# Kernel optimization log

Measured on AMD Instinct MI355X. Metric: run time of the kernel, lower is better.

Reference implementation:

```python
import jax, jax.numpy as jnp
import numpy as np

B, N, D, H, O = 4096, 128, 64, 256, 128  # batch, memory_size, memory_dim, controller_dim, output_size


def setup_inputs() -> dict:
    key = jax.random.key(0)
    ks = jax.random.split(key, 20)
    s = 0.05
    inp = {
        "x": jax.random.normal(ks[0], (B, O), jnp.float32),
        "memory": jax.random.normal(ks[1], (B, N, D), jnp.float32),
        "h": jax.random.normal(ks[2], (B, H), jnp.float32),
        "c": jax.random.normal(ks[3], (B, H), jnp.float32),
        # LSTMCell params (torch layout: gates ordered i, f, g, o; input = x||read_vec of width O+D)
        "W_ih": jax.random.normal(ks[4], (4 * H, O + D), jnp.float32) * s,
        "W_hh": jax.random.normal(ks[5], (4 * H, H), jnp.float32) * s,
        "b_ih": jax.random.normal(ks[6], (4 * H,), jnp.float32) * s,
        "b_hh": jax.random.normal(ks[7], (4 * H,), jnp.float32) * s,
        "W_read": jax.random.normal(ks[8], (N, H), jnp.float32) * s,
        "b_read": jax.random.normal(ks[9], (N,), jnp.float32) * s,
        "W_write": jax.random.normal(ks[10], (N, H), jnp.float32) * s,
        "b_write": jax.random.normal(ks[11], (N,), jnp.float32) * s,
        "W_erase": jax.random.normal(ks[12], (D, H), jnp.float32) * s,
        "b_erase": jax.random.normal(ks[13], (D,), jnp.float32) * s,
        "W_add": jax.random.normal(ks[14], (D, H), jnp.float32) * s,
        "b_add": jax.random.normal(ks[15], (D,), jnp.float32) * s,
        "W_out": jax.random.normal(ks[16], (O, H + D), jnp.float32) * s,
        "b_out": jax.random.normal(ks[17], (O,), jnp.float32) * s,
    }
    return inp


def reference(x, memory, h, c, W_ih, W_hh, b_ih, b_hh, W_read, b_read,
              W_write, b_write, W_erase, b_erase, W_add, b_add, W_out, b_out):
    # read: softmax attention over memory rows, addressed by previous hidden state
    read_w = jax.nn.softmax(h @ W_read.T + b_read, axis=-1)          # [B, N]
    read_vec = jnp.einsum("bn,bnd->bd", read_w, memory)               # [B, D]

    # LSTMCell step (torch gate order: i, f, g, o)
    ctrl_in = jnp.concatenate([x, read_vec], axis=-1)                 # [B, O+D]
    gates = ctrl_in @ W_ih.T + b_ih + h @ W_hh.T + b_hh               # [B, 4H]
    i, f, g, o = jnp.split(gates, 4, axis=-1)
    i, f, o = jax.nn.sigmoid(i), jax.nn.sigmoid(f), jax.nn.sigmoid(o)
    g = jnp.tanh(g)
    c_new = f * c + i * g
    h_new = o * jnp.tanh(c_new)

    # write: outer-product erase/add update
    write_w = jax.nn.softmax(h_new @ W_write.T + b_write, axis=-1)    # [B, N]
    erase = jax.nn.sigmoid(h_new @ W_erase.T + b_erase)               # [B, D]
    add = jnp.tanh(h_new @ W_add.T + b_add)                           # [B, D]
    ww = write_w[:, :, None]                                          # [B, N, 1]
    mem_new = memory * (1.0 - ww * erase[:, None, :]) + ww * add[:, None, :]

    out = jnp.concatenate([h_new, read_vec], axis=-1) @ W_out.T + b_out  # [B, O]
    return (out, mem_new, h_new, c_new)
```

## Files before the change

kernel.cpp:

```cpp
#include <hip/hip_runtime.h>
#include <math.h>


typedef __attribute__((ext_vector_type(8))) short bf16x8;
typedef __attribute__((ext_vector_type(4))) float f32x4;
typedef __attribute__((ext_vector_type(4))) unsigned short us4;

#define MFMA16(a, b, c) __builtin_amdgcn_mfma_f32_16x16x32_bf16(a, b, c, 0, 0, 0)
#define GLL16(gp, lp) __builtin_amdgcn_global_load_lds( \
    (const __attribute__((address_space(1))) void*)(gp), \
    (__attribute__((address_space(3))) void*)(lp), 16, 0, 0)
#define SW(row, s) ((s) ^ ((row) & 3))

__device__ __forceinline__ float sigf(float v) { return 1.f / (1.f + __expf(-v)); }

__device__ __forceinline__ unsigned short f2bf(float f) {
    unsigned u = __builtin_bit_cast(unsigned, f);
    u = (u + 0x7FFFu + ((u >> 16) & 1u)) >> 16;
    return (unsigned short)u;
}

__global__ __launch_bounds__(256) void p_pack(
    const float* __restrict__ Wih, const float* __restrict__ Whh,
    const float* __restrict__ bih, const float* __restrict__ bhh,
    const float* __restrict__ Wr, const float* __restrict__ Ww,
    const float* __restrict__ We, const float* __restrict__ Wa,
    const float* __restrict__ bw, const float* __restrict__ be,
    const float* __restrict__ ba, const float* __restrict__ Wo,
    const float* __restrict__ x, const float* __restrict__ h,
    unsigned short* __restrict__ Wg, float* __restrict__ bsum,
    unsigned short* __restrict__ Wr_b, unsigned short* __restrict__ Wh_b,
    float* __restrict__ bh_b, unsigned short* __restrict__ Wo_b,
    unsigned short* __restrict__ Ag)
{
    int idx = blockIdx.x * 256 + threadIdx.x;
    int stride = gridDim.x * 256;
    for (int i = idx; i < 1024 * 448; i += stride) {
        int r = i / 448, cc = i - r * 448;
        float v = (cc < 192) ? Wih[(size_t)r * 192 + cc] : Whh[(size_t)r * 256 + (cc - 192)];
        Wg[i] = f2bf(v);
    }
    for (int i = idx; i < 1024; i += stride) bsum[i] = bih[i] + bhh[i];
    for (int i = idx; i < 128 * 256; i += stride) Wr_b[i] = f2bf(Wr[i]);
    for (int i = idx; i < 256 * 256; i += stride) {
        int r = i >> 8, cc = i & 255;
        float v = (r < 128) ? Ww[(size_t)r * 256 + cc]
                : (r < 192) ? We[(size_t)(r - 128) * 256 + cc]
                            : Wa[(size_t)(r - 192) * 256 + cc];
        Wh_b[i] = f2bf(v);
    }
    for (int i = idx; i < 256; i += stride)
        bh_b[i] = (i < 128) ? bw[i] : (i < 192 ? be[i - 128] : ba[i - 192]);
    for (int i = idx; i < 128 * 320; i += stride) Wo_b[i] = f2bf(Wo[i]);
    for (int i = idx; i < 4096 * 96; i += stride) {
        int row = i / 96, j = i - row * 96;
        float4 v = (j < 32) ? ((const float4*)(x + (size_t)row * 128))[j]
                            : ((const float4*)(h + (size_t)row * 256))[j - 32];
        us4 o = { f2bf(v.x), f2bf(v.y), f2bf(v.z), f2bf(v.w) };
        int col = (j < 32) ? j * 4 : 192 + (j - 32) * 4;
        *(us4*)(Ag + (size_t)row * 448 + col) = o;
    }
}

__global__ __launch_bounds__(128) void k1_read_attn(
    const unsigned short* __restrict__ Ag, const unsigned short* __restrict__ Wr_b,
    const float* __restrict__ br, float* __restrict__ read_w)
{
    __shared__ unsigned short As[32 * 32];
    __shared__ unsigned short Bs[128 * 32];
    int t = threadIdx.x;
    int wid = t >> 6, lane = t & 63;
    int cl = lane & 15, ks = lane >> 4;
    int b0 = blockIdx.x * 32;

    int arow = t >> 2;
    const unsigned short* aSrc = Ag + (size_t)(b0 + arow) * 448 + 192 + SW(arow, t & 3) * 8;
    unsigned short* aDst = As + wid * 512;
    const unsigned short* bSrc[4];
    unsigned short* bDst[4];
#pragma unroll
    for (int J = 0; J < 4; ++J) {
        int rJ = J * 32 + (t >> 2);
        bSrc[J] = Wr_b + (size_t)rJ * 256 + SW(rJ, t & 3) * 8;
        bDst[J] = Bs + J * 1024 + wid * 512;
    }

    int mr = wid * 16 + cl;
    int aOff = mr * 32 + SW(mr, ks) * 8;
    int bOff[8];
#pragma unroll
    for (int f = 0; f < 8; ++f) { int br_ = f * 16 + cl; bOff[f] = br_ * 32 + SW(br_, ks) * 8; }

    f32x4 acc[8] = {};
    for (int kc = 0; kc < 8; ++kc) {
        __syncthreads();
        GLL16(aSrc, aDst);
#pragma unroll
        for (int J = 0; J < 4; ++J) GLL16(bSrc[J], bDst[J]);
        aSrc += 32;
#pragma unroll
        for (int J = 0; J < 4; ++J) bSrc[J] += 32;
        __syncthreads();
        bf16x8 a = *(const bf16x8*)(As + aOff);
#pragma unroll
        for (int f = 0; f < 8; ++f)
            acc[f] = MFMA16(a, *(const bf16x8*)(Bs + bOff[f]), acc[f]);
    }

    float bb[8];
#pragma unroll
    for (int f = 0; f < 8; ++f) bb[f] = br[f * 16 + cl];
#pragma unroll
    for (int r = 0; r < 4; ++r) {
        int row = b0 + wid * 16 + ks * 4 + r;
        float v[8];
#pragma unroll
        for (int f = 0; f < 8; ++f) v[f] = acc[f][r] + bb[f];
        float m = v[0];
#pragma unroll
        for (int f = 1; f < 8; ++f) m = fmaxf(m, v[f]);
#pragma unroll
        for (int mk = 8; mk >= 1; mk >>= 1) m = fmaxf(m, __shfl_xor(m, mk));
        float s = 0.f;
#pragma unroll
        for (int f = 0; f < 8; ++f) { v[f] = __expf(v[f] - m); s += v[f]; }
#pragma unroll
        for (int mk = 8; mk >= 1; mk >>= 1) s += __shfl_xor(s, mk);
        float inv = 1.f / s;
#pragma unroll
        for (int f = 0; f < 8; ++f)
            read_w[(size_t)row * 128 + f * 16 + cl] = v[f] * inv;
    }
}

__global__ __launch_bounds__(256) void k2_read_vec(
    const float* __restrict__ mem, const float* __restrict__ read_w,
    unsigned short* __restrict__ Ag, unsigned short* __restrict__ Aout)
{
    __shared__ float part[16][68];
    int t = threadIdx.x;
    int b = blockIdx.x;
    int np = t >> 4, d4 = t & 15;
    const float4* m4 = (const float4*)(mem + (size_t)b * 8192);
    float4 acc = make_float4(0.f, 0.f, 0.f, 0.f);
#pragma unroll
    for (int j = 0; j < 8; ++j) {
        int n = np + 16 * j;
        float w = read_w[(size_t)b * 128 + n];
        float4 mv = m4[t + 256 * j];
        acc.x += w * mv.x; acc.y += w * mv.y; acc.z += w * mv.z; acc.w += w * mv.w;
    }
    part[np][d4 * 4 + 0] = acc.x; part[np][d4 * 4 + 1] = acc.y;
    part[np][d4 * 4 + 2] = acc.z; part[np][d4 * 4 + 3] = acc.w;
    __syncthreads();
    if (t < 64) {
        float s = 0.f;
#pragma unroll
        for (int q = 0; q < 16; ++q) s += part[q][t];
        unsigned short bv = f2bf(s);
        Ag[(size_t)b * 448 + 128 + t] = bv;
        Aout[(size_t)b * 320 + 256 + t] = bv;
    }
}

__global__ __launch_bounds__(256) void k3_gates_mfma(
    const unsigned short* __restrict__ Ag, const unsigned short* __restrict__ Wg,
    const float* __restrict__ bsum, const float* __restrict__ c,
    float* __restrict__ h_new, float* __restrict__ c_new,
    unsigned short* __restrict__ Aout)
{
    __shared__ unsigned short As[64 * 32];
    __shared__ unsigned short Bs[256 * 32];
    int t = threadIdx.x;
    int wid = t >> 6, lane = t & 63;
    int cl = lane & 15, ks = lane >> 4;
    int b0 = blockIdx.x * 64;
    int u0 = blockIdx.y * 64;

    int arow = t >> 2;
    const unsigned short* aSrc = Ag + (size_t)(b0 + arow) * 448 + SW(arow, t & 3) * 8;
    unsigned short* aDst = As + wid * 512;
    const unsigned short* bSrc[4];
    unsigned short* bDst[4];
#pragma unroll
    for (int j = 0; j < 4; ++j) {
        int i = j * 256 + t;
        int rl = i >> 2;
        int g = rl >> 6, u = rl & 63;
        bSrc[j] = Wg + (size_t)(g * 256 + u0 + u) * 448 + SW(rl, t & 3) * 8;
        bDst[j] = Bs + (j * 256 + wid * 64) * 8;
    }

    int aOff[4];
#pragma unroll
    for (int rf = 0; rf < 4; ++rf) {
        int mr = rf * 16 + cl;
        aOff[rf] = mr * 32 + SW(mr, ks) * 8;
    }
    int bOff[4];
#pragma unroll
    for (int g = 0; g < 4; ++g) {
        int br_ = g * 64 + wid * 16 + cl;
        bOff[g] = br_ * 32 + SW(br_, ks) * 8;
    }

    f32x4 acc[4][4] = {};
    for (int kc = 0; kc < 14; ++kc) {
        __syncthreads();
        GLL16(aSrc, aDst);
        GLL16(bSrc[0], bDst[0]); GLL16(bSrc[1], bDst[1]);
        GLL16(bSrc[2], bDst[2]); GLL16(bSrc[3], bDst[3]);
        aSrc += 32;
#pragma unroll
        for (int j = 0; j < 4; ++j) bSrc[j] += 32;
        __syncthreads();
        bf16x8 a[4], b[4];
#pragma unroll
        for (int rf = 0; rf < 4; ++rf) a[rf] = *(const bf16x8*)(As + aOff[rf]);
#pragma unroll
        for (int g = 0; g < 4; ++g) b[g] = *(const bf16x8*)(Bs + bOff[g]);
#pragma unroll
        for (int rf = 0; rf < 4; ++rf)
#pragma unroll
            for (int g = 0; g < 4; ++g)
                acc[rf][g] = MFMA16(a[rf], b[g], acc[rf][g]);
    }

    int unit = u0 + wid * 16 + cl;
    float bi = bsum[unit], bf_ = bsum[256 + unit];
    float bg = bsum[512 + unit], bo_ = bsum[768 + unit];
#pragma unroll
    for (int rf = 0; rf < 4; ++rf) {
#pragma unroll
        for (int r = 0; r < 4; ++r) {
            int row = b0 + rf * 16 + ks * 4 + r;
            float iv = sigf(acc[rf][0][r] + bi);
            float fv = sigf(acc[rf][1][r] + bf_);
            float gv = tanhf(acc[rf][2][r] + bg);
            float ov = sigf(acc[rf][3][r] + bo_);
            float cv = fv * c[(size_t)row * 256 + unit] + iv * gv;
            float hv = ov * tanhf(cv);
            c_new[(size_t)row * 256 + unit] = cv;
            h_new[(size_t)row * 256 + unit] = hv;
            Aout[(size_t)row * 320 + unit] = f2bf(hv);
        }
    }
}

__global__ __launch_bounds__(256) void k46_heads_out(
    const unsigned short* __restrict__ Aout, const unsigned short* __restrict__ Wh_b,
    const unsigned short* __restrict__ Wo_b, const float* __restrict__ bh_b,
    const float* __restrict__ bo, float* __restrict__ write_w,
    float* __restrict__ erase, float* __restrict__ addv, float* __restrict__ outp)
{
    __shared__ unsigned short As[32 * 32];
    __shared__ unsigned short Bh[256 * 32];
    __shared__ unsigned short Bo[128 * 32];
    int t = threadIdx.x;
    int wid = t >> 6, lane = t & 63;
    int cl = lane & 15, ks = lane >> 4;
    int rf = wid >> 1, ch = wid & 1;
    int b0 = blockIdx.x * 32;

    int arow = t >> 2;
    const unsigned short* aSrc = Aout + (size_t)(b0 + (arow & 31)) * 320 + SW(arow & 31, t & 3) * 8;
    unsigned short* aDst = As + (wid & 1) * 512;
    const unsigned short* bhSrc[4];
    unsigned short* bhDst[4];
#pragma unroll
    for (int j = 0; j < 4; ++j) {
        int rl = (j * 256 + t) >> 2;
        bhSrc[j] = Wh_b + (size_t)rl * 256 + SW(rl, t & 3) * 8;
        bhDst[j] = Bh + (j * 256 + wid * 64) * 8;
    }
    const unsigned short* boSrc[2];
    unsigned short* boDst[2];
#pragma unroll
    for (int j = 0; j < 2; ++j) {
        int rj = j * 64 + (t >> 2);
        boSrc[j] = Wo_b + (size_t)rj * 320 + SW(rj, t & 3) * 8;
        boDst[j] = Bo + j * 2048 + wid * 512;
    }

    int mr = rf * 16 + cl;
    int aOff = mr * 32 + SW(mr, ks) * 8;
    int bOffH[8], bOffO[4];
#pragma unroll
    for (int f = 0; f < 8; ++f) { int br_ = (ch * 8 + f) * 16 + cl; bOffH[f] = br_ * 32 + SW(br_, ks) * 8; }
#pragma unroll
    for (int f = 0; f < 4; ++f) { int br_ = (ch * 4 + f) * 16 + cl; bOffO[f] = br_ * 32 + SW(br_, ks) * 8; }

    f32x4 accH[8] = {};
    f32x4 accO[4] = {};
    for (int kc = 0; kc < 10; ++kc) {
        __syncthreads();
        if (t < 128) GLL16(aSrc, aDst);
        if (kc < 8) {
            GLL16(bhSrc[0], bhDst[0]); GLL16(bhSrc[1], bhDst[1]);
            GLL16(bhSrc[2], bhDst[2]); GLL16(bhSrc[3], bhDst[3]);
        }
        GLL16(boSrc[0], boDst[0]); GLL16(boSrc[1], boDst[1]);
        aSrc += 32;
#pragma unroll
        for (int j = 0; j < 4; ++j) bhSrc[j] += 32;
#pragma unroll
        for (int j = 0; j < 2; ++j) boSrc[j] += 32;
        __syncthreads();
        bf16x8 a = *(const bf16x8*)(As + aOff);
        if (kc < 8) {
#pragma unroll
            for (int f = 0; f < 8; ++f)
                accH[f] = MFMA16(a, *(const bf16x8*)(Bh + bOffH[f]), accH[f]);
        }
#pragma unroll
        for (int f = 0; f < 4; ++f)
            accO[f] = MFMA16(a, *(const bf16x8*)(Bo + bOffO[f]), accO[f]);
    }

    float bbh[8], bbo[4];
#pragma unroll
    for (int f = 0; f < 8; ++f) bbh[f] = bh_b[(ch * 8 + f) * 16 + cl];
#pragma unroll
    for (int f = 0; f < 4; ++f) bbo[f] = bo[ch * 64 + f * 16 + cl];

#pragma unroll
    for (int r = 0; r < 4; ++r) {
        int row = b0 + rf * 16 + ks * 4 + r;
        if (ch == 0) {
            float v[8];
#pragma unroll
            for (int f = 0; f < 8; ++f) v[f] = accH[f][r] + bbh[f];
            float m = v[0];
#pragma unroll
            for (int f = 1; f < 8; ++f) m = fmaxf(m, v[f]);
#pragma unroll
            for (int mk = 8; mk >= 1; mk >>= 1) m = fmaxf(m, __shfl_xor(m, mk));
            float s = 0.f;
#pragma unroll
            for (int f = 0; f < 8; ++f) { v[f] = __expf(v[f] - m); s += v[f]; }
#pragma unroll
            for (int mk = 8; mk >= 1; mk >>= 1) s += __shfl_xor(s, mk);
            float inv = 1.f / s;
#pragma unroll
            for (int f = 0; f < 8; ++f)
                write_w[(size_t)row * 128 + f * 16 + cl] = v[f] * inv;
        } else {
#pragma unroll
            for (int f = 0; f < 4; ++f)
                erase[(size_t)row * 64 + f * 16 + cl] = sigf(accH[f][r] + bbh[f]);
#pragma unroll
            for (int f = 4; f < 8; ++f)
                addv[(size_t)row * 64 + (f - 4) * 16 + cl] = tanhf(accH[f][r] + bbh[f]);
        }
#pragma unroll
        for (int f = 0; f < 4; ++f)
            outp[(size_t)row * 128 + ch * 64 + f * 16 + cl] = accO[f][r] + bbo[f];
    }
}

__global__ __launch_bounds__(256) void k5_mem_update(
    const float* __restrict__ mem, const float* __restrict__ write_w,
    const float* __restrict__ erase, const float* __restrict__ addv,
    float* __restrict__ mem_new)
{
    int t = threadIdx.x; int b = blockIdx.x;
    int np = t >> 4, d0 = (t & 15) * 4;
    const f32x4* m4 = (const f32x4*)(mem + (size_t)b * 8192);
    f32x4* o4 = (f32x4*)(mem_new + (size_t)b * 8192);
    f32x4 e4 = *(const f32x4*)(erase + (size_t)b * 64 + d0);
    f32x4 a4 = *(const f32x4*)(addv + (size_t)b * 64 + d0);
#pragma unroll
    for (int j = 0; j < 8; ++j) {
        int n = np + 16 * j;
        float w = write_w[(size_t)b * 128 + n];
        f32x4 m = m4[t + 256 * j];
        f32x4 r;
        r[0] = m[0] * (1.f - w * e4[0]) + w * a4[0];
        r[1] = m[1] * (1.f - w * e4[1]) + w * a4[1];
        r[2] = m[2] * (1.f - w * e4[2]) + w * a4[2];
        r[3] = m[3] * (1.f - w * e4[3]) + w * a4[3];
        __builtin_nontemporal_store(r, &o4[t + 256 * j]);
    }
}

extern "C" void kernel_launch(void* const* d_in, const int* in_sizes, int n_in,
                              void* d_out, int out_size, void* d_ws, size_t ws_size,
                              hipStream_t stream)
{
    const float* x    = (const float*)d_in[0];
    const float* mem  = (const float*)d_in[1];
    const float* h    = (const float*)d_in[2];
    const float* c    = (const float*)d_in[3];
    const float* Wih  = (const float*)d_in[4];
    const float* Whh  = (const float*)d_in[5];
    const float* bih  = (const float*)d_in[6];
    const float* bhh  = (const float*)d_in[7];
    const float* Wr   = (const float*)d_in[8];
    const float* br   = (const float*)d_in[9];
    const float* Ww   = (const float*)d_in[10];
    const float* bw   = (const float*)d_in[11];
    const float* We   = (const float*)d_in[12];
    const float* be   = (const float*)d_in[13];
    const float* Wa   = (const float*)d_in[14];
    const float* ba   = (const float*)d_in[15];
    const float* Wo   = (const float*)d_in[16];
    const float* bo   = (const float*)d_in[17];

    float* out     = (float*)d_out;
    float* mem_new = out + 524288;
    float* h_new   = out + 34078720;
    float* c_new   = out + 35127296;

    float* ws      = (float*)d_ws;
    float* read_w  = ws;
    float* write_w = ws + 524288;
    float* erase   = ws + 1048576;
    float* addv    = ws + 1310720;
    float* bsum    = ws + 1572864;
    float* bh_b    = ws + 1573888;
    unsigned short* ub   = (unsigned short*)(ws + 1574144);
    unsigned short* Ag   = ub;
    unsigned short* Aout = ub + 1835008;
    unsigned short* Wg   = ub + 3145728;
    unsigned short* Wr_b = ub + 3604480;
    unsigned short* Wh_b = ub + 3637248;
    unsigned short* Wo_b = ub + 3702784;

    p_pack<<<512, 256, 0, stream>>>(Wih, Whh, bih, bhh, Wr, Ww, We, Wa, bw, be, ba, Wo,
                                    x, h, Wg, bsum, Wr_b, Wh_b, bh_b, Wo_b, Ag);
    k1_read_attn<<<128, 128, 0, stream>>>(Ag, Wr_b, br, read_w);
    k2_read_vec<<<4096, 256, 0, stream>>>(mem, read_w, Ag, Aout);
    k3_gates_mfma<<<dim3(64, 4), 256, 0, stream>>>(Ag, Wg, bsum, c, h_new, c_new, Aout);
    k46_heads_out<<<128, 256, 0, stream>>>(Aout, Wh_b, Wo_b, bh_b, bo,
                                           write_w, erase, addv, out);
    k5_mem_update<<<4096, 256, 0, stream>>>(mem, write_w, erase, addv, mem_new);
}
```

Baseline: 110.6 us.

## Fuse six kernels into three: prep+read attention, gates, heads+memory update

```diff
diff --git a/kernel.cpp b/kernel.cpp
--- a/kernel.cpp
+++ b/kernel.cpp
@@ -20,20 +20,32 @@
     return (unsigned short)u;
 }
 
-__global__ __launch_bounds__(256) void p_pack(
+__global__ __launch_bounds__(256) void kA_prep(
     const float* __restrict__ Wih, const float* __restrict__ Whh,
     const float* __restrict__ bih, const float* __restrict__ bhh,
-    const float* __restrict__ Wr, const float* __restrict__ Ww,
-    const float* __restrict__ We, const float* __restrict__ Wa,
-    const float* __restrict__ bw, const float* __restrict__ be,
-    const float* __restrict__ ba, const float* __restrict__ Wo,
-    const float* __restrict__ x, const float* __restrict__ h,
+    const float* __restrict__ Wr, const float* __restrict__ br,
+    const float* __restrict__ Ww, const float* __restrict__ We,
+    const float* __restrict__ Wa, const float* __restrict__ bw,
+    const float* __restrict__ be, const float* __restrict__ ba,
+    const float* __restrict__ Wo, const float* __restrict__ x,
+    const float* __restrict__ h, const float* __restrict__ mem,
     unsigned short* __restrict__ Wg, float* __restrict__ bsum,
-    unsigned short* __restrict__ Wr_b, unsigned short* __restrict__ Wh_b,
-    float* __restrict__ bh_b, unsigned short* __restrict__ Wo_b,
-    unsigned short* __restrict__ Ag)
+    unsigned short* __restrict__ Wh_b, float* __restrict__ bh_b,
+    unsigned short* __restrict__ Wo_b, unsigned short* __restrict__ Ag,
+    unsigned short* __restrict__ Aout)
 {
-    int idx = blockIdx.x * 256 + threadIdx.x;
+    __shared__ unsigned short As[16 * 32];
+    __shared__ unsigned short Bs[128 * 32];
+    __shared__ float sc[16][128];
+    __shared__ float wL[16][128];
+    __shared__ float part[16][68];
+
+    int t = threadIdx.x;
+    int wid = t >> 6, lane = t & 63;
+    int cl = lane & 15, ks = lane >> 4;
+    int b0 = blockIdx.x * 16;
+
+    int idx = blockIdx.x * 256 + t;
     int stride = gridDim.x * 256;
     for (int i = idx; i < 1024 * 448; i += stride) {
         int r = i / 448, cc = i - r * 448;
@@ -41,7 +53,6 @@
         Wg[i] = f2bf(v);
     }
     for (int i = idx; i < 1024; i += stride) bsum[i] = bih[i] + bhh[i];
-    for (int i = idx; i < 128 * 256; i += stride) Wr_b[i] = f2bf(Wr[i]);
     for (int i = idx; i < 256 * 256; i += stride) {
         int r = i >> 8, cc = i & 255;
         float v = (r < 128) ? Ww[(size_t)r * 256 + cc]
@@ -60,110 +71,102 @@
         int col = (j < 32) ? j * 4 : 192 + (j - 32) * 4;
         *(us4*)(Ag + (size_t)row * 448 + col) = o;
     }
-}
-
-__global__ __launch_bounds__(128) void k1_read_attn(
-    const unsigned short* __restrict__ Ag, const unsigned short* __restrict__ Wr_b,
-    const float* __restrict__ br, float* __restrict__ read_w)
-{
-    __shared__ unsigned short As[32 * 32];
-    __shared__ unsigned short Bs[128 * 32];
-    int t = threadIdx.x;
-    int wid = t >> 6, lane = t & 63;
-    int cl = lane & 15, ks = lane >> 4;
-    int b0 = blockIdx.x * 32;
-
-    int arow = t >> 2;
-    const unsigned short* aSrc = Ag + (size_t)(b0 + arow) * 448 + 192 + SW(arow, t & 3) * 8;
-    unsigned short* aDst = As + wid * 512;
-    const unsigned short* bSrc[4];
-    unsigned short* bDst[4];
-#pragma unroll
-    for (int J = 0; J < 4; ++J) {
-        int rJ = J * 32 + (t >> 2);
-        bSrc[J] = Wr_b + (size_t)rJ * 256 + SW(rJ, t & 3) * 8;
-        bDst[J] = Bs + J * 1024 + wid * 512;
-    }
-
-    int mr = wid * 16 + cl;
-    int aOff = mr * 32 + SW(mr, ks) * 8;
-    int bOff[8];
-#pragma unroll
-    for (int f = 0; f < 8; ++f) { int br_ = f * 16 + cl; bOff[f] = br_ * 32 + SW(br_, ks) * 8; }
-
-    f32x4 acc[8] = {};
+
+    int aOff = cl * 32 + SW(cl, ks) * 8;
+    int bOff[4];
+#pragma unroll
+    for (int f = 0; f < 4; ++f) {
+        int br_ = (wid * 4 + f) * 16 + cl;
+        bOff[f] = br_ * 32 + SW(br_, ks) * 8;
+    }
+    f32x4 acc[4] = {};
     for (int kc = 0; kc < 8; ++kc) {
         __syncthreads();
-        GLL16(aSrc, aDst);
-#pragma unroll
-        for (int J = 0; J < 4; ++J) GLL16(bSrc[J], bDst[J]);
-        aSrc += 32;
-#pragma unroll
-        for (int J = 0; J < 4; ++J) bSrc[J] += 32;
-        __syncthreads();
-        bf16x8 a = *(const bf16x8*)(As + aOff);
-#pragma unroll
-        for (int f = 0; f < 8; ++f)
-            acc[f] = MFMA16(a, *(const bf16x8*)(Bs + bOff[f]), acc[f]);
-    }
-
-    float bb[8];
-#pragma unroll
-    for (int f = 0; f < 8; ++f) bb[f] = br[f * 16 + cl];
-#pragma unroll
-    for (int r = 0; r < 4; ++r) {
-        int row = b0 + wid * 16 + ks * 4 + r;
+        {
+            int row = t >> 4, k0 = (t & 15) * 2;
+            float2 hv = *(const float2*)(h + (size_t)(b0 + row) * 256 + kc * 32 + k0);
+            unsigned pk = (unsigned)f2bf(hv.x) | ((unsigned)f2bf(hv.y) << 16);
+            *(unsigned*)(As + row * 32 + SW(row, k0 >> 3) * 8 + (k0 & 7)) = pk;
+        }
+        {
+            int row = t >> 1, k0 = (t & 1) * 16;
+            const float4* wp = (const float4*)(Wr + (size_t)row * 256 + kc * 32 + k0);
+            float4 w0 = wp[0], w1 = wp[1], w2 = wp[2], w3 = wp[3];
+            us4 p0 = { f2bf(w0.x), f2bf(w0.y), f2bf(w0.z), f2bf(w0.w) };
+            us4 p1 = { f2bf(w1.x), f2bf(w1.y), f2bf(w1.z), f2bf(w1.w) };
+            us4 p2 = { f2bf(w2.x), f2bf(w2.y), f2bf(w2.z), f2bf(w2.w) };
+            us4 p3 = { f2bf(w3.x), f2bf(w3.y), f2bf(w3.z), f2bf(w3.w) };
+            int g0 = k0 >> 3;
+            unsigned short* basep = Bs + row * 32;
+            *(us4*)(basep + SW(row, g0) * 8)     = p0;
+            *(us4*)(basep + SW(row, g0) * 8 + 4) = p1;
+            *(us4*)(basep + SW(row, g0 + 1) * 8)     = p2;
+            *(us4*)(basep + SW(row, g0 + 1) * 8 + 4) = p3;
+        }
+        __syncthreads();
+        if (wid < 2) {
+            bf16x8 a = *(const bf16x8*)(As + aOff);
+#pragma unroll
+            for (int f = 0; f < 4; ++f)
+                acc[f] = MFMA16(a, *(const bf16x8*)(Bs + bOff[f]), acc[f]);
+        }
+    }
+    if (wid < 2) {
+#pragma unroll
+        for (int f = 0; f < 4; ++f)
+#pragma unroll
+            for (int r = 0; r < 4; ++r)
+                sc[ks * 4 + r][(wid * 4 + f) * 16 + cl] = acc[f][r];
+    }
+    __syncthreads();
+    {
+        int row = t >> 4, l = t & 15;
         float v[8];
 #pragma unroll
-        for (int f = 0; f < 8; ++f) v[f] = acc[f][r] + bb[f];
+        for (int j = 0; j < 8; ++j) v[j] = sc[row][l + 16 * j] + br[l + 16 * j];
         float m = v[0];
 #pragma unroll
-        for (int f = 1; f < 8; ++f) m = fmaxf(m, v[f]);
+        for (int j = 1; j < 8; ++j) m = fmaxf(m, v[j]);
 #pragma unroll
         for (int mk = 8; mk >= 1; mk >>= 1) m = fmaxf(m, __shfl_xor(m, mk));
         float s = 0.f;
 #pragma unroll
-        for (int f = 0; f < 8; ++f) { v[f] = __expf(v[f] - m); s += v[f]; }
+        for (int j = 0; j < 8; ++j) { v[j] = __expf(v[j] - m); s += v[j]; }
 #pragma unroll
         for (int mk = 8; mk >= 1; mk >>= 1) s += __shfl_xor(s, mk);
         float inv = 1.f / s;
 #pragma unroll
-        for (int f = 0; f < 8; ++f)
-            read_w[(size_t)row * 128 + f * 16 + cl] = v[f] * inv;
+        for (int j = 0; j < 8; ++j) wL[row][l + 16 * j] = v[j] * inv;
+    }
+    __syncthreads();
+
+    int np = t >> 4, d4 = t & 15;
+    for (int r = 0; r < 16; ++r) {
+        int row = b0 + r;
+        const f32x4* m4 = (const f32x4*)(mem + (size_t)row * 8192);
+        f32x4 a4 = { 0.f, 0.f, 0.f, 0.f };
+#pragma unroll
+        for (int j = 0; j < 8; ++j) {
+            float w = wL[r][np + 16 * j];
+            f32x4 mv = m4[t + 256 * j];
+            a4 += w * mv;
+        }
+        part[np][d4 * 4 + 0] = a4[0]; part[np][d4 * 4 + 1] = a4[1];
+        part[np][d4 * 4 + 2] = a4[2]; part[np][d4 * 4 + 3] = a4[3];
+        __syncthreads();
+        if (t < 64) {
+            float s = 0.f;
+#pragma unroll
+            for (int q = 0; q < 16; ++q) s += part[q][t];
+            unsigned short bv = f2bf(s);
+            Ag[(size_t)row * 448 + 128 + t] = bv;
+            Aout[(size_t)row * 320 + 256 + t] = bv;
+        }
+        __syncthreads();
     }
 }
 
-__global__ __launch_bounds__(256) void k2_read_vec(
-    const float* __restrict__ mem, const float* __restrict__ read_w,
-    unsigned short* __restrict__ Ag, unsigned short* __restrict__ Aout)
-{
-    __shared__ float part[16][68];
-    int t = threadIdx.x;
-    int b = blockIdx.x;
-    int np = t >> 4, d4 = t & 15;
-    const float4* m4 = (const float4*)(mem + (size_t)b * 8192);
-    float4 acc = make_float4(0.f, 0.f, 0.f, 0.f);
-#pragma unroll
-    for (int j = 0; j < 8; ++j) {
-        int n = np + 16 * j;
-        float w = read_w[(size_t)b * 128 + n];
-        float4 mv = m4[t + 256 * j];
-        acc.x += w * mv.x; acc.y += w * mv.y; acc.z += w * mv.z; acc.w += w * mv.w;
-    }
-    part[np][d4 * 4 + 0] = acc.x; part[np][d4 * 4 + 1] = acc.y;
-    part[np][d4 * 4 + 2] = acc.z; part[np][d4 * 4 + 3] = acc.w;
-    __syncthreads();
-    if (t < 64) {
-        float s = 0.f;
-#pragma unroll
-        for (int q = 0; q < 16; ++q) s += part[q][t];
-        unsigned short bv = f2bf(s);
-        Ag[(size_t)b * 448 + 128 + t] = bv;
-        Aout[(size_t)b * 320 + 256 + t] = bv;
-    }
-}
-
-__global__ __launch_bounds__(256) void k3_gates_mfma(
+__global__ __launch_bounds__(256) void kB_gates(
     const unsigned short* __restrict__ Ag, const unsigned short* __restrict__ Wg,
     const float* __restrict__ bsum, const float* __restrict__ c,
     float* __restrict__ h_new, float* __restrict__ c_new,
@@ -184,8 +187,7 @@
     unsigned short* bDst[4];
 #pragma unroll
     for (int j = 0; j < 4; ++j) {
-        int i = j * 256 + t;
-        int rl = i >> 2;
+        int rl = (j * 256 + t) >> 2;
         int g = rl >> 6, u = rl & 63;
         bSrc[j] = Wg + (size_t)(g * 256 + u0 + u) * 448 + SW(rl, t & 3) * 8;
         bDst[j] = Bs + (j * 256 + wid * 64) * 8;
@@ -247,24 +249,26 @@
     }
 }
 
-__global__ __launch_bounds__(256) void k46_heads_out(
+__global__ __launch_bounds__(256) void kC_heads_out_mem(
     const unsigned short* __restrict__ Aout, const unsigned short* __restrict__ Wh_b,
     const unsigned short* __restrict__ Wo_b, const float* __restrict__ bh_b,
-    const float* __restrict__ bo, float* __restrict__ write_w,
-    float* __restrict__ erase, float* __restrict__ addv, float* __restrict__ outp)
+    const float* __restrict__ bo, const float* __restrict__ mem,
+    float* __restrict__ outp, float* __restrict__ mem_new)
 {
-    __shared__ unsigned short As[32 * 32];
+    __shared__ unsigned short As[16 * 32];
     __shared__ unsigned short Bh[256 * 32];
     __shared__ unsigned short Bo[128 * 32];
+    __shared__ float sc[16][256];
+    __shared__ __align__(16) float wL[16][128];
+    __shared__ __align__(16) float eL[16][64];
+    __shared__ __align__(16) float aL[16][64];
+
     int t = threadIdx.x;
     int wid = t >> 6, lane = t & 63;
     int cl = lane & 15, ks = lane >> 4;
-    int rf = wid >> 1, ch = wid & 1;
-    int b0 = blockIdx.x * 32;
-
-    int arow = t >> 2;
-    const unsigned short* aSrc = Aout + (size_t)(b0 + (arow & 31)) * 320 + SW(arow & 31, t & 3) * 8;
-    unsigned short* aDst = As + (wid & 1) * 512;
+    int b0 = blockIdx.x * 16;
+
+    const unsigned short* aSrc = Aout + (size_t)(b0 + (lane >> 2)) * 320 + SW(lane >> 2, lane & 3) * 8;
     const unsigned short* bhSrc[4];
     unsigned short* bhDst[4];
 #pragma unroll
@@ -282,19 +286,18 @@
         boDst[j] = Bo + j * 2048 + wid * 512;
     }
 
-    int mr = rf * 16 + cl;
-    int aOff = mr * 32 + SW(mr, ks) * 8;
-    int bOffH[8], bOffO[4];
-#pragma unroll
-    for (int f = 0; f < 8; ++f) { int br_ = (ch * 8 + f) * 16 + cl; bOffH[f] = br_ * 32 + SW(br_, ks) * 8; }
-#pragma unroll
-    for (int f = 0; f < 4; ++f) { int br_ = (ch * 4 + f) * 16 + cl; bOffO[f] = br_ * 32 + SW(br_, ks) * 8; }
-
-    f32x4 accH[8] = {};
-    f32x4 accO[4] = {};
+    int aOff = cl * 32 + SW(cl, ks) * 8;
+    int bOffH[4], bOffO[2];
+#pragma unroll
+    for (int f = 0; f < 4; ++f) { int br_ = (wid * 4 + f) * 16 + cl; bOffH[f] = br_ * 32 + SW(br_, ks) * 8; }
+#pragma unroll
+    for (int f = 0; f < 2; ++f) { int br_ = (wid * 2 + f) * 16 + cl; bOffO[f] = br_ * 32 + SW(br_, ks) * 8; }
+
+    f32x4 accH[4] = {};
+    f32x4 accO[2] = {};
     for (int kc = 0; kc < 10; ++kc) {
         __syncthreads();
-        if (t < 128) GLL16(aSrc, aDst);
+        if (t < 64) GLL16(aSrc, As);
         if (kc < 8) {
             GLL16(bhSrc[0], bhDst[0]); GLL16(bhSrc[1], bhDst[1]);
             GLL16(bhSrc[2], bhDst[2]); GLL16(bhSrc[3], bhDst[3]);
@@ -309,77 +312,74 @@
         bf16x8 a = *(const bf16x8*)(As + aOff);
         if (kc < 8) {
 #pragma unroll
-            for (int f = 0; f < 8; ++f)
+            for (int f = 0; f < 4; ++f)
                 accH[f] = MFMA16(a, *(const bf16x8*)(Bh + bOffH[f]), accH[f]);
         }
 #pragma unroll
-        for (int f = 0; f < 4; ++f)
+        for (int f = 0; f < 2; ++f)
             accO[f] = MFMA16(a, *(const bf16x8*)(Bo + bOffO[f]), accO[f]);
     }
 
-    float bbh[8], bbo[4];
-#pragma unroll
-    for (int f = 0; f < 8; ++f) bbh[f] = bh_b[(ch * 8 + f) * 16 + cl];
-#pragma unroll
-    for (int f = 0; f < 4; ++f) bbo[f] = bo[ch * 64 + f * 16 + cl];
-
-#pragma unroll
-    for (int r = 0; r < 4; ++r) {
-        int row = b0 + rf * 16 + ks * 4 + r;
-        if (ch == 0) {
-            float v[8];
-#pragma unroll
-            for (int f = 0; f < 8; ++f) v[f] = accH[f][r] + bbh[f];
-            float m = v[0];
-#pragma unroll
-            for (int f = 1; f < 8; ++f) m = fmaxf(m, v[f]);
-#pragma unroll
-            for (int mk = 8; mk >= 1; mk >>= 1) m = fmaxf(m, __shfl_xor(m, mk));
-            float s = 0.f;
-#pragma unroll
-            for (int f = 0; f < 8; ++f) { v[f] = __expf(v[f] - m); s += v[f]; }
-#pragma unroll
-            for (int mk = 8; mk >= 1; mk >>= 1) s += __shfl_xor(s, mk);
-            float inv = 1.f / s;
-#pragma unroll
-            for (int f = 0; f < 8; ++f)
-                write_w[(size_t)row * 128 + f * 16 + cl] = v[f] * inv;
-        } else {
-#pragma unroll
-            for (int f = 0; f < 4; ++f)
-                erase[(size_t)row * 64 + f * 16 + cl] = sigf(accH[f][r] + bbh[f]);
-#pragma unroll
-            for (int f = 4; f < 8; ++f)
-                addv[(size_t)row * 64 + (f - 4) * 16 + cl] = tanhf(accH[f][r] + bbh[f]);
-        }
-#pragma unroll
-        for (int f = 0; f < 4; ++f)
-            outp[(size_t)row * 128 + ch * 64 + f * 16 + cl] = accO[f][r] + bbo[f];
-    }
-}
-
-__global__ __launch_bounds__(256) void k5_mem_update(
-    const float* __restrict__ mem, const float* __restrict__ write_w,
-    const float* __restrict__ erase, const float* __restrict__ addv,
-    float* __restrict__ mem_new)
-{
-    int t = threadIdx.x; int b = blockIdx.x;
-    int np = t >> 4, d0 = (t & 15) * 4;
-    const f32x4* m4 = (const f32x4*)(mem + (size_t)b * 8192);
-    f32x4* o4 = (f32x4*)(mem_new + (size_t)b * 8192);
-    f32x4 e4 = *(const f32x4*)(erase + (size_t)b * 64 + d0);
-    f32x4 a4 = *(const f32x4*)(addv + (size_t)b * 64 + d0);
-#pragma unroll
-    for (int j = 0; j < 8; ++j) {
-        int n = np + 16 * j;
-        float w = write_w[(size_t)b * 128 + n];
-        f32x4 m = m4[t + 256 * j];
-        f32x4 r;
-        r[0] = m[0] * (1.f - w * e4[0]) + w * a4[0];
-        r[1] = m[1] * (1.f - w * e4[1]) + w * a4[1];
-        r[2] = m[2] * (1.f - w * e4[2]) + w * a4[2];
-        r[3] = m[3] * (1.f - w * e4[3]) + w * a4[3];
-        __builtin_nontemporal_store(r, &o4[t + 256 * j]);
+#pragma unroll
+    for (int f = 0; f < 4; ++f) {
+        int col = (wid * 4 + f) * 16 + cl;
+        float bb = bh_b[col];
+#pragma unroll
+        for (int r = 0; r < 4; ++r)
+            sc[ks * 4 + r][col] = accH[f][r] + bb;
+    }
+#pragma unroll
+    for (int f = 0; f < 2; ++f) {
+        int col = (wid * 2 + f) * 16 + cl;
+        float bb = bo[col];
+#pragma unroll
+        for (int r = 0; r < 4; ++r)
+            outp[(size_t)(b0 + ks * 4 + r) * 128 + col] = accO[f][r] + bb;
+    }
+    __syncthreads();
+    {
+        int row = t >> 4, l = t & 15;
+        float v[8];
+#pragma unroll
+        for (int j = 0; j < 8; ++j) v[j] = sc[row][l + 16 * j];
+        float m = v[0];
+#pragma unroll
+        for (int j = 1; j < 8; ++j) m = fmaxf(m, v[j]);
+#pragma unroll
+        for (int mk = 8; mk >= 1; mk >>= 1) m = fmaxf(m, __shfl_xor(m, mk));
+        float s = 0.f;
+#pragma unroll
+        for (int j = 0; j < 8; ++j) { v[j] = __expf(v[j] - m); s += v[j]; }
+#pragma unroll
+        for (int mk = 8; mk >= 1; mk >>= 1) s += __shfl_xor(s, mk);
+        float inv = 1.f / s;
+#pragma unroll
+        for (int j = 0; j < 8; ++j) wL[row][l + 16 * j] = v[j] * inv;
+#pragma unroll
+        for (int j = 0; j < 4; ++j) eL[row][l + 16 * j] = sigf(sc[row][128 + l + 16 * j]);
+#pragma unroll
+        for (int j = 0; j < 4; ++j) aL[row][l + 16 * j] = tanhf(sc[row][192 + l + 16 * j]);
+    }
+    __syncthreads();
+
+    int np = t >> 4, d4 = t & 15;
+    for (int r = 0; r < 16; ++r) {
+        int row = b0 + r;
+        const f32x4* m4 = (const f32x4*)(mem + (size_t)row * 8192);
+        f32x4* o4 = (f32x4*)(mem_new + (size_t)row * 8192);
+        f32x4 e4 = *(const f32x4*)&eL[r][d4 * 4];
+        f32x4 a4 = *(const f32x4*)&aL[r][d4 * 4];
+#pragma unroll
+        for (int j = 0; j < 8; ++j) {
+            float w = wL[r][np + 16 * j];
+            f32x4 m = m4[t + 256 * j];
+            f32x4 rr;
+            rr[0] = m[0] * (1.f - w * e4[0]) + w * a4[0];
+            rr[1] = m[1] * (1.f - w * e4[1]) + w * a4[1];
+            rr[2] = m[2] * (1.f - w * e4[2]) + w * a4[2];
+            rr[3] = m[3] * (1.f - w * e4[3]) + w * a4[3];
+            __builtin_nontemporal_store(rr, &o4[t + 256 * j]);
+        }
     }
 }
 
@@ -411,27 +411,18 @@
     float* h_new   = out + 34078720;
     float* c_new   = out + 35127296;
 
-    float* ws      = (float*)d_ws;
-    float* read_w  = ws;
-    float* write_w = ws + 524288;
-    float* erase   = ws + 1048576;
-    float* addv    = ws + 1310720;
-    float* bsum    = ws + 1572864;
-    float* bh_b    = ws + 1573888;
-    unsigned short* ub   = (unsigned short*)(ws + 1574144);
+    float* ws   = (float*)d_ws;
+    float* bsum = ws;
+    float* bh_b = ws + 1024;
+    unsigned short* ub   = (unsigned short*)(ws + 1280);
     unsigned short* Ag   = ub;
     unsigned short* Aout = ub + 1835008;
     unsigned short* Wg   = ub + 3145728;
-    unsigned short* Wr_b = ub + 3604480;
-    unsigned short* Wh_b = ub + 3637248;
-    unsigned short* Wo_b = ub + 3702784;
-
-    p_pack<<<512, 256, 0, stream>>>(Wih, Whh, bih, bhh, Wr, Ww, We, Wa, bw, be, ba, Wo,
-                                    x, h, Wg, bsum, Wr_b, Wh_b, bh_b, Wo_b, Ag);
-    k1_read_attn<<<128, 128, 0, stream>>>(Ag, Wr_b, br, read_w);
-    k2_read_vec<<<4096, 256, 0, stream>>>(mem, read_w, Ag, Aout);
-    k3_gates_mfma<<<dim3(64, 4), 256, 0, stream>>>(Ag, Wg, bsum, c, h_new, c_new, Aout);
-    k46_heads_out<<<128, 256, 0, stream>>>(Aout, Wh_b, Wo_b, bh_b, bo,
-                                           write_w, erase, addv, out);
-    k5_mem_update<<<4096, 256, 0, stream>>>(mem, write_w, erase, addv, mem_new);
+    unsigned short* Wh_b = ub + 3604480;
+    unsigned short* Wo_b = ub + 3670016;
+
+    kA_prep<<<256, 256, 0, stream>>>(Wih, Whh, bih, bhh, Wr, br, Ww, We, Wa, bw, be, ba,
+                                     Wo, x, h, mem, Wg, bsum, Wh_b, bh_b, Wo_b, Ag, Aout);
+    kB_gates<<<dim3(64, 4), 256, 0, stream>>>(Ag, Wg, bsum, c, h_new, c_new, Aout);
+    kC_heads_out_mem<<<256, 256, 0, stream>>>(Aout, Wh_b, Wo_b, bh_b, bo, mem, out, mem_new);
 }
```

After: 106.6 us. 3.5% less time.
